# Kernel tuning notes

Measured on AMD Instinct MI355X. Metric: run time of the kernel, lower is better.

The kernel has to match this reference:

```python
import jax, jax.numpy as jnp
import numpy as np

B, L, D, H, MEM, POL = 32, 256, 768, 12, 384, 3
DK = D // H
ALPHA, BETA, GAMA = 1.0, 0.25, 0.1


def _forward(sequence_output, pooled_output, adj_reshape, src_mask, aspect_mask,
             ln_g, ln_b, wq, bq, wk, bk, wd, bd, weight_m, bias_m,
             wa0, ba0, wa1, ba1, ws0, bs0, ws1, bs1, affine1, affine2, wc, bc):
    b, l, d = sequence_output.shape
    h = weight_m.shape[0]
    dk = d // h

    # custom LayerNorm (torch std is unbiased, ddof=1)
    mu = sequence_output.mean(-1, keepdims=True)
    sd = jnp.std(sequence_output, axis=-1, keepdims=True, ddof=1)
    x = ln_g * (sequence_output - mu) / (sd + 1e-6) + ln_b  # gcn_inputs (dropout = eval identity)

    aspect_outs = x * aspect_mask[:, :, None]

    # multi-head projections  [B,H,L,dk]
    q = (x @ wq + bq).reshape(b, l, h, dk).transpose(0, 2, 1, 3)
    k = (x @ wk + bk).reshape(b, l, h, dk).transpose(0, 2, 1, 3)
    asp = aspect_outs @ wd + bd                       # [B,L,dk]
    asp = jnp.broadcast_to(asp[:, None], (b, h, l, dk))

    # aspect-conditioned scores: tanh(aspect @ W_m @ K^T + b_m)   [B,H,L,L]
    asps = jnp.tanh(jnp.einsum('bhld,hde,bhme->bhlm', asp, weight_m, k) + bias_m[0])
    avg = asps.sum(axis=-2) / l                       # [B,H,L]

    # fusion overwrite: for each aspect index idx, row idx and col idx <- avg.
    # Sequential loop semantics (ascending idx, row-then-col) collapse to:
    #   both aspect (i,j): value = avg[min(i,j)];  row-only: avg[j];  col-only: avg[i]
    is_asp = aspect_mask > 0                          # [B,L]
    rowm = is_asp[:, None, :, None]
    colm = is_asp[:, None, None, :]
    avg_i = avg[..., :, None]                         # [B,H,L,1]
    avg_j = avg[..., None, :]                         # [B,H,1,L]
    ge = (jnp.arange(l)[:, None] >= jnp.arange(l)[None, :])  # i>=j -> min=j
    both_val = jnp.where(ge, avg_j, avg_i)
    aspect_scores = jnp.where(rowm & colm, both_val,
                      jnp.where(rowm, avg_j,
                        jnp.where(colm, avg_i, asps)))

    # standard scaled-dot attention
    scores = jnp.einsum('bhld,bhmd->bhlm', q, k) / jnp.sqrt(jnp.float32(dk))
    scores = jnp.where(src_mask[:, None, None, :] == 0, -1e9, scores)
    s_attn = jax.nn.softmax(scores, axis=-1)          # dropout = eval identity

    aspect_score_avg = aspect_scores.mean(axis=1)     # [B,L,L]
    adj_s = s_attn.mean(axis=1)                       # [B,L,L]

    eye = jnp.eye(l, dtype=adj_s.dtype)
    adj_s = adj_s * (1.0 - eye) + eye                 # zero diag then add identity
    adj_s = src_mask[:, :, None] * adj_s

    adj_r = jnp.exp(ALPHA * adj_reshape)
    dist_mask = aspect_score_avg > BETA
    adj_r = jnp.where(dist_mask, 1.0, adj_r)
    adj_ag = adj_r * aspect_score_avg

    log_p = jax.nn.log_softmax(adj_ag, axis=-1)
    log_q = jax.nn.log_softmax(adj_s, axis=-1)
    q_t = jnp.exp(log_q)
    kl = jnp.sum(q_t * (log_q - log_p))
    kl_loss = jnp.exp(-1.0 * kl * GAMA)

    denom_s = adj_s.sum(axis=2, keepdims=True) + 1.0
    denom_ag = adj_ag.sum(axis=2, keepdims=True) + 1.0

    out_ag, out_s = x, x
    was = [(wa0, ba0), (wa1, ba1)]
    wss = [(ws0, bs0), (ws1, bs1)]
    for li in range(2):
        g_ag = jax.nn.relu(((adj_ag @ out_ag) @ was[li][0] + was[li][1]) / denom_ag)
        g_s = jax.nn.relu(((adj_s @ out_s) @ wss[li][0] + wss[li][1]) / denom_s)
        A1 = jax.nn.softmax(jnp.einsum('bld,de,bme->blm', g_ag, affine1, g_s), axis=-1)
        A2 = jax.nn.softmax(jnp.einsum('bld,de,bme->blm', g_s, affine2, g_ag), axis=-1)
        out_ag = A1 @ g_s
        out_s = A2 @ g_ag   # gcn_drop = eval identity

    asp_wn = aspect_mask.sum(axis=1, keepdims=True)   # [B,1]
    m = aspect_mask[:, :, None]
    outputs1 = (out_ag * m).sum(axis=1) / asp_wn      # [B,MEM]
    outputs2 = (out_s * m).sum(axis=1) / asp_wn

    final = jnp.concatenate([outputs1, outputs2, pooled_output], axis=-1) @ wc + bc
    return final, kl_loss


def setup_inputs() -> dict:
    key = jax.random.key(0)
    ks = jax.random.split(key, 16)
    s = 0.02
    pos = jnp.arange(L)
    start = 5 + (jnp.arange(B) % 16)
    aspect_mask = ((pos[None, :] >= start[:, None]) & (pos[None, :] < start[:, None] + 3)).astype(jnp.float32)
    f32 = jnp.float32
    return {
        'sequence_output': jax.random.normal(ks[0], (B, L, D), f32),
        'pooled_output': jax.random.normal(ks[1], (B, D), f32),
        'adj_reshape': jax.random.uniform(ks[2], (B, L, L), f32),
        'src_mask': jnp.ones((B, L), f32),
        'aspect_mask': aspect_mask,
        'ln_g': jnp.ones((D,), f32), 'ln_b': jnp.zeros((D,), f32),
        'wq': jax.random.normal(ks[3], (D, D), f32) * s, 'bq': jnp.zeros((D,), f32),
        'wk': jax.random.normal(ks[4], (D, D), f32) * s, 'bk': jnp.zeros((D,), f32),
        'wd': jax.random.normal(ks[5], (D, DK), f32) * s, 'bd': jnp.zeros((DK,), f32),
        'weight_m': jax.random.normal(ks[6], (H, DK, DK), f32) * s,
        'bias_m': jnp.zeros((1,), f32),
        'wa0': jax.random.normal(ks[7], (D, MEM), f32) * s, 'ba0': jnp.zeros((MEM,), f32),
        'wa1': jax.random.normal(ks[8], (MEM, MEM), f32) * s, 'ba1': jnp.zeros((MEM,), f32),
        'ws0': jax.random.normal(ks[9], (D, MEM), f32) * s, 'bs0': jnp.zeros((MEM,), f32),
        'ws1': jax.random.normal(ks[10], (MEM, MEM), f32) * s, 'bs1': jnp.zeros((MEM,), f32),
        'affine1': jax.random.normal(ks[11], (MEM, MEM), f32) * s,
        'affine2': jax.random.normal(ks[12], (MEM, MEM), f32) * s,
        'wc': jax.random.normal(ks[13], (2 * D, POL), f32) * s, 'bc': jnp.zeros((POL,), f32),
    }


def reference(sequence_output, pooled_output, adj_reshape, src_mask, aspect_mask,
              ln_g, ln_b, wq, bq, wk, bk, wd, bd, weight_m, bias_m,
              wa0, ba0, wa1, ba1, ws0, bs0, ws1, bs1, affine1, affine2, wc, bc):
    return _forward(sequence_output, pooled_output, adj_reshape, src_mask, aspect_mask,
                    ln_g, ln_b, wq, bq, wk, bk, wd, bd, weight_m, bias_m,
                    wa0, ba0, wa1, ba1, ws0, bs0, ws1, bs1, affine1, affine2, wc, bc)
```

## Files before the change

### kernel.cpp

```cpp
#include <hip/hip_runtime.h>

#define B_ 32
#define L_ 256
#define D_ 768
#define H_ 12
#define DK_ 64
#define MEM_ 384

typedef __attribute__((ext_vector_type(8))) short bfrag8;
typedef __attribute__((ext_vector_type(8))) unsigned short us8;
typedef __attribute__((ext_vector_type(4))) float f32x4;

__device__ inline unsigned short f2bf(float f) {
  unsigned u = __float_as_uint(f);
  return (unsigned short)((u + 0x7fffu + ((u >> 16) & 1u)) >> 16);
}
__device__ inline float bf2f(unsigned short u) {
  return __uint_as_float(((unsigned)u) << 16);
}
__device__ inline float tanh_fast(float x) {
  x = fminf(fmaxf(x, -30.f), 30.f);
  float e = __expf(2.f * x);
  return (e - 1.f) * __builtin_amdgcn_rcpf(e + 1.f);
}
__device__ inline void gload_lds16(const unsigned short* g, unsigned short* l) {
  __builtin_amdgcn_global_load_lds(
      (__attribute__((address_space(1))) void*)(g),
      (__attribute__((address_space(3))) void*)(l), 16, 0, 0);
}

__device__ inline float waveRedSum(float v) {
#pragma unroll
  for (int o = 32; o; o >>= 1) v += __shfl_xor(v, o, 64);
  return v;
}
__device__ inline float waveRedMax(float v) {
#pragma unroll
  for (int o = 32; o; o >>= 1) v = fmaxf(v, __shfl_xor(v, o, 64));
  return v;
}
__device__ inline float blkRedSum(float v, float* red) {
  v = waveRedSum(v);
  int w = threadIdx.x >> 6;
  __syncthreads();
  if ((threadIdx.x & 63) == 0) red[w] = v;
  __syncthreads();
  return red[0] + red[1] + red[2] + red[3];
}
__device__ inline float blkRedMax(float v, float* red) {
  v = waveRedMax(v);
  int w = threadIdx.x >> 6;
  __syncthreads();
  if ((threadIdx.x & 63) == 0) red[w] = v;
  __syncthreads();
  return fmaxf(fmaxf(red[0], red[1]), fmaxf(red[2], red[3]));
}

__global__ __launch_bounds__(256) void prep_kernel(
    const float* __restrict__ seq, const float* __restrict__ lng,
    const float* __restrict__ lnb, float* __restrict__ xout,
    unsigned short* __restrict__ xbf,
    const float* __restrict__ wq, unsigned short* __restrict__ wqT,
    const float* __restrict__ wk, unsigned short* __restrict__ wkT,
    const float* __restrict__ wa0, unsigned short* __restrict__ wa0T,
    const float* __restrict__ ws0, unsigned short* __restrict__ ws0T,
    const float* __restrict__ wa1, unsigned short* __restrict__ wa1T,
    const float* __restrict__ ws1, unsigned short* __restrict__ ws1T,
    const float* __restrict__ aff1, unsigned short* __restrict__ aff1T,
    const float* __restrict__ aff2, unsigned short* __restrict__ aff2T,
    const float* __restrict__ wd, unsigned short* __restrict__ wdT,
    const float* __restrict__ wm, unsigned short* __restrict__ wmT) {
  int bid = blockIdx.x;
  if (bid >= 600) {
    long row = bid - 600;
    const float* p = seq + row * D_;
    float v[3];
#pragma unroll
    for (int i = 0; i < 3; ++i) v[i] = p[threadIdx.x + i * 256];
    __shared__ float red[4];
    float s = v[0] + v[1] + v[2];
    s = blkRedSum(s, red);
    float mu = s * (1.f / D_);
    float ss = 0.f;
#pragma unroll
    for (int i = 0; i < 3; ++i) { float d = v[i] - mu; ss += d * d; }
    ss = blkRedSum(ss, red);
    float sd = sqrtf(ss * (1.f / (D_ - 1)));
    float inv = 1.f / (sd + 1e-6f);
#pragma unroll
    for (int i = 0; i < 3; ++i) {
      int c = threadIdx.x + i * 256;
      float o = lng[c] * (v[i] - mu) * inv + lnb[c];
      xout[row * D_ + c] = o;
      xbf[row * D_ + c] = f2bf(o);
    }
    return;
  }
  const float* src; unsigned short* dst; int Rr, Cc, tIdx;
  if (bid < 144)      { src = wq;   dst = wqT;   Rr = 768; Cc = 768; tIdx = bid; }
  else if (bid < 288) { src = wk;   dst = wkT;   Rr = 768; Cc = 768; tIdx = bid - 144; }
  else if (bid < 360) { src = wa0;  dst = wa0T;  Rr = 768; Cc = 384; tIdx = bid - 288; }
  else if (bid < 432) { src = ws0;  dst = ws0T;  Rr = 768; Cc = 384; tIdx = bid - 360; }
  else if (bid < 468) { src = wa1;  dst = wa1T;  Rr = 384; Cc = 384; tIdx = bid - 432; }
  else if (bid < 504) { src = ws1;  dst = ws1T;  Rr = 384; Cc = 384; tIdx = bid - 468; }
  else if (bid < 540) { src = aff1; dst = aff1T; Rr = 384; Cc = 384; tIdx = bid - 504; }
  else if (bid < 576) { src = aff2; dst = aff2T; Rr = 384; Cc = 384; tIdx = bid - 540; }
  else if (bid < 588) { src = wd;   dst = wdT;   Rr = 768; Cc = 64;  tIdx = bid - 576; }
  else { int h = bid - 588; src = wm + h * 4096; dst = wmT + h * 4096; Rr = 64; Cc = 64; tIdx = 0; }
  __shared__ float tile[64][65];
  int nx = Cc >> 6;
  int c0 = (tIdx % nx) * 64, r0 = (tIdx / nx) * 64;
  int tx = threadIdx.x & 63, ty = threadIdx.x >> 6;
#pragma unroll
  for (int i = 0; i < 16; ++i)
    tile[ty + i * 4][tx] = src[(long)(r0 + ty + i * 4) * Cc + c0 + tx];
  __syncthreads();
#pragma unroll
  for (int i = 0; i < 16; ++i)
    dst[(long)(c0 + ty + i * 4) * Rr + r0 + tx] = f2bf(tile[tx][ty + i * 4]);
}

template <int MR>
__global__ __launch_bounds__(256) void gemm_bb(
    const unsigned short* __restrict__ A, const unsigned short* __restrict__ Bt,
    float* __restrict__ C, unsigned short* __restrict__ Cbf,
    unsigned short* __restrict__ CT,
    int M, int N, int K, long sA, long sB, long sC, long sCT,
    const float* __restrict__ bias, const float* __restrict__ rowDiv, int relu,
    const unsigned short* __restrict__ A2, const unsigned short* __restrict__ Bt2,
    float* __restrict__ C2, unsigned short* __restrict__ Cbf2,
    unsigned short* __restrict__ CT2,
    const float* __restrict__ bias2, const float* __restrict__ rowDiv2, int zsplit,
    int GX, int GZ, int gmode) {
  constexpr int MFRAG = MR / 32;
  constexpr int RW = MR / 2;
  constexpr int ASH = MR * 32;
  constexpr int BUFS = ASH + 4096;
  constexpr int TSH = 64 * (MR + 8);
  constexpr int SMN = (2 * BUFS > TSH) ? 2 * BUFS : TSH;
  __shared__ alignas(16) unsigned short smem[SMN];
  const int tid = threadIdx.x;
  int dtot = blockIdx.x;
  int xcd = dtot & 7, rrg = dtot >> 3;
  int gsz = GX * GZ;
  if (gmode == 1) gsz = blockIdx.y;
  int bn, bm, bz;
  if (gmode == 0) {
    int ul = rrg / gsz, j = rrg % gsz;
    bm = ul * 8 + xcd;
    bz = j / GX;
    bn = j % GX;
  } else {
    int gsz2 = GX * GZ;
    int ul = rrg / gsz2, j = rrg % gsz2;
    bz = ul * 8 + xcd;
    bm = j / GX;
    bn = j % GX;
  }
  const unsigned short* Ap = A; const unsigned short* Btp = Bt;
  float* Cp = C; unsigned short* Cbp = Cbf; unsigned short* CTp = CT;
  const float* biasp = bias; const float* rowDivp = rowDiv;
  if (zsplit > 0 && bz >= zsplit) {
    bz -= zsplit;
    Ap = A2; Btp = Bt2; Cp = C2; Cbp = Cbf2; CTp = CT2; biasp = bias2; rowDivp = rowDiv2;
  }
  Ap += (long)bz * sA; Btp += (long)bz * sB;
  if (Cp) Cp += (long)bz * sC;
  if (Cbp) Cbp += (long)bz * sC;
  if (CTp) CTp += (long)bz * sCT;

  f32x4 acc[MFRAG][4] = {};
  const int l = tid & 63, w = tid >> 6;
  const int wr = w >> 1, wc = w & 1;
  const int lr = l & 15, sg = l >> 4;

  const int rc = l >> 2;
  const int sslot = (l & 3) ^ ((rc >> 1) & 3);
  const unsigned short* gA0 = Ap + (long)(bm * MR + w * 16 + rc) * K + sslot * 8;
  const unsigned short* gA1 = (MR == 128)
      ? Ap + (long)(bm * MR + (w + 4) * 16 + rc) * K + sslot * 8 : nullptr;
  const unsigned short* gB0 = Btp + (long)(bn * 128 + w * 16 + rc) * K + sslot * 8;
  const unsigned short* gB1 = Btp + (long)(bn * 128 + (w + 4) * 16 + rc) * K + sslot * 8;
  const int stA0 = w * 512, stA1 = (w + 4) * 512;
  const int stB0 = ASH + w * 512, stB1 = ASH + (w + 4) * 512;

  const int swz = (sg ^ ((lr >> 1) & 3)) * 8;
  int aoff[MFRAG], boff[4];
#pragma unroll
  for (int m = 0; m < MFRAG; ++m) aoff[m] = (wr * RW + m * 16 + lr) * 32 + swz;
#pragma unroll
  for (int n = 0; n < 4; ++n) boff[n] = ASH + (wc * 64 + n * 16 + lr) * 32 + swz;

  const int nt = K >> 5;
  gload_lds16(gA0, smem + stA0);
  if (MR == 128) gload_lds16(gA1, smem + stA1);
  gload_lds16(gB0, smem + stB0);
  gload_lds16(gB1, smem + stB1);

  for (int t = 0; t < nt; ++t) {
    const int cur = (t & 1) * BUFS;
    if (t + 1 < nt) {
      const int nxt = ((t + 1) & 1) * BUFS;
      const int k1 = (t + 1) << 5;
      gload_lds16(gA0 + k1, smem + nxt + stA0);
      if (MR == 128) gload_lds16(gA1 + k1, smem + nxt + stA1);
      gload_lds16(gB0 + k1, smem + nxt + stB0);
      gload_lds16(gB1 + k1, smem + nxt + stB1);
      if constexpr (MR == 128)
        asm volatile("s_waitcnt vmcnt(4)" ::: "memory");
      else
        asm volatile("s_waitcnt vmcnt(3)" ::: "memory");
    } else {
      asm volatile("s_waitcnt vmcnt(0)" ::: "memory");
    }
    __builtin_amdgcn_s_barrier();
    asm volatile("" ::: "memory");
    bfrag8 af[MFRAG], bf[4];
#pragma unroll
    for (int m = 0; m < MFRAG; ++m) af[m] = *(const bfrag8*)(smem + cur + aoff[m]);
#pragma unroll
    for (int n = 0; n < 4; ++n) bf[n] = *(const bfrag8*)(smem + cur + boff[n]);
#pragma unroll
    for (int m = 0; m < MFRAG; ++m)
#pragma unroll
      for (int n = 0; n < 4; ++n)
        acc[m][n] = __builtin_amdgcn_mfma_f32_16x16x32_bf16(af[m], bf[n], acc[m][n], 0, 0, 0);
    asm volatile("" ::: "memory");
    __builtin_amdgcn_s_barrier();
    asm volatile("" ::: "memory");
  }

  if (Cp || Cbp) {
#pragma unroll
    for (int m = 0; m < MFRAG; ++m) {
#pragma unroll
      for (int r = 0; r < 4; ++r) {
        int row = bm * MR + wr * RW + m * 16 + (l >> 4) * 4 + r;
        float rd = rowDivp ? 1.f / rowDivp[(long)bz * M + row] : 1.f;
#pragma unroll
        for (int n = 0; n < 4; ++n) {
          int col = bn * 128 + wc * 64 + n * 16 + lr;
          float v = acc[m][n][r];
          if (biasp) v += biasp[col];
          v *= rd;
          if (relu) v = fmaxf(v, 0.f);
          if (Cp) Cp[(long)row * N + col] = v;
          if (Cbp) Cbp[(long)row * N + col] = f2bf(v);
        }
      }
    }
  }
  if (CT) {
    auto Ts = (unsigned short(*)[MR + 8])smem;
#pragma unroll
    for (int ch = 0; ch < 2; ++ch) {
      __syncthreads();
      if (wc == ch) {
#pragma unroll
        for (int m = 0; m < MFRAG; ++m) {
#pragma unroll
          for (int r = 0; r < 4; ++r) {
            int rowl = wr * RW + m * 16 + (l >> 4) * 4 + r;
            float rd = rowDivp ? 1.f / rowDivp[(long)bz * M + bm * MR + rowl] : 1.f;
#pragma unroll
            for (int n = 0; n < 4; ++n) {
              int col = bn * 128 + wc * 64 + n * 16 + lr;
              float v = acc[m][n][r];
              if (biasp) v += biasp[col];
              v *= rd;
              if (relu) v = fmaxf(v, 0.f);
              Ts[n * 16 + lr][rowl] = f2bf(v);
            }
          }
        }
      }
      __syncthreads();
      int trow = tid >> 2, tc = (tid & 3) * (MR / 4);
      int colg = bn * 128 + ch * 64 + trow;
      int rowg = bm * MR + tc;
      unsigned short* dp = CTp + (long)(rowg >> 8) * sCT + (long)colg * 256 + (rowg & 255);
#pragma unroll
      for (int j = 0; j < MR / 32; ++j)
        *(us8*)(dp + j * 8) = *(const us8*)&Ts[trow][tc + j * 8];
    }
  }
}

__global__ __launch_bounds__(256) void attn_asp(
    const unsigned short* __restrict__ qbf, const unsigned short* __restrict__ kbf,
    const float* __restrict__ srcm,
    float* __restrict__ part0, float* __restrict__ part1,
    const unsigned short* __restrict__ xbf, const unsigned short* __restrict__ wdT,
    const float* __restrict__ amask, const float* __restrict__ bd,
    unsigned short* __restrict__ aspbf) {
  int t = threadIdx.x;
  int w = t >> 6, l = t & 63;
  int lr = l & 15, kg = (l >> 4) * 8;
  if (blockIdx.x >= 1024) {
    int l0 = (blockIdx.x - 1024) << 4;
    const unsigned short* ap = xbf + (long)(l0 + lr) * D_ + kg;
    const unsigned short* bp = wdT + (long)(w * 16 + lr) * D_ + kg;
    f32x4 acc = {};
#pragma unroll
    for (int k0 = 0; k0 < D_; k0 += 32) {
      bfrag8 af = *(const bfrag8*)(ap + k0);
      bfrag8 bf = *(const bfrag8*)(bp + k0);
      acc = __builtin_amdgcn_mfma_f32_16x16x32_bf16(af, bf, acc, 0, 0, 0);
    }
    int col = w * 16 + lr;
#pragma unroll
    for (int r = 0; r < 4; ++r) {
      int row = l0 + (l >> 4) * 4 + r;
      float v = acc[r] * amask[row] + bd[col];
      aspbf[(long)row * DK_ + col] = f2bf(v);
    }
    return;
  }
  int d = blockIdx.x;
  int b = (d & 7) + 8 * ((d >> 3) & 3);
  int rest = d >> 5;
  int l0 = (rest & 15) << 4;
  int half = rest >> 4;
  int rbase = (l >> 4) * 4;
  __shared__ float red[3][2][16][4];
  float acc[4][4] = {};
  float cmv[4];
#pragma unroll
  for (int ct = 0; ct < 4; ++ct) cmv[ct] = srcm[b * L_ + w * 64 + ct * 16 + lr];

  const int hp0 = half * 3;
  const long qrow = (long)b * L_ + l0 + lr;
  const unsigned short* apq = qbf + qrow * D_ + hp0 * 128 + kg;
  bfrag8 a00 = *(const bfrag8*)apq;
  bfrag8 a01 = *(const bfrag8*)(apq + 32);
  bfrag8 a10 = *(const bfrag8*)(apq + 64);
  bfrag8 a11 = *(const bfrag8*)(apq + 96);
  bfrag8 kv[4][4];
#pragma unroll
  for (int ct = 0; ct < 4; ++ct) {
    const unsigned short* bp =
        kbf + ((long)b * L_ + w * 64 + ct * 16 + lr) * D_ + hp0 * 128 + kg;
    kv[ct][0] = *(const bfrag8*)bp;
    kv[ct][1] = *(const bfrag8*)(bp + 32);
    kv[ct][2] = *(const bfrag8*)(bp + 64);
    kv[ct][3] = *(const bfrag8*)(bp + 96);
  }

#pragma unroll 1
  for (int ph = 0; ph < 3; ++ph) {
    float sv0[4][4], sv1[4][4];
#pragma unroll
    for (int ct = 0; ct < 4; ++ct) {
      f32x4 c0 = {}, c1 = {};
      c0 = __builtin_amdgcn_mfma_f32_16x16x32_bf16(a00, kv[ct][0], c0, 0, 0, 0);
      c0 = __builtin_amdgcn_mfma_f32_16x16x32_bf16(a01, kv[ct][1], c0, 0, 0, 0);
      c1 = __builtin_amdgcn_mfma_f32_16x16x32_bf16(a10, kv[ct][2], c1, 0, 0, 0);
      c1 = __builtin_amdgcn_mfma_f32_16x16x32_bf16(a11, kv[ct][3], c1, 0, 0, 0);
#pragma unroll
      for (int r = 0; r < 4; ++r) { sv0[ct][r] = c0[r]; sv1[ct][r] = c1[r]; }
    }
    if (ph < 2) {
      const unsigned short* apn = qbf + qrow * D_ + (hp0 + ph + 1) * 128 + kg;
      a00 = *(const bfrag8*)apn;
      a01 = *(const bfrag8*)(apn + 32);
      a10 = *(const bfrag8*)(apn + 64);
      a11 = *(const bfrag8*)(apn + 96);
#pragma unroll
      for (int ct = 0; ct < 4; ++ct) {
        const unsigned short* bp =
            kbf + ((long)b * L_ + w * 64 + ct * 16 + lr) * D_ + (hp0 + ph + 1) * 128 + kg;
        kv[ct][0] = *(const bfrag8*)bp;
        kv[ct][1] = *(const bfrag8*)(bp + 32);
        kv[ct][2] = *(const bfrag8*)(bp + 64);
        kv[ct][3] = *(const bfrag8*)(bp + 96);
      }
    }
#pragma unroll
    for (int ct = 0; ct < 4; ++ct) {
      bool msk = (cmv[ct] == 0.f);
#pragma unroll
      for (int r = 0; r < 4; ++r) {
        sv0[ct][r] = __expf(msk ? -1e9f : sv0[ct][r] * 0.125f);
        sv1[ct][r] = __expf(msk ? -1e9f : sv1[ct][r] * 0.125f);
      }
    }
#pragma unroll
    for (int r = 0; r < 4; ++r) {
      float s0 = sv0[0][r] + sv0[1][r] + sv0[2][r] + sv0[3][r];
      float s1 = sv1[0][r] + sv1[1][r] + sv1[2][r] + sv1[3][r];
#pragma unroll
      for (int o = 1; o < 16; o <<= 1) {
        s0 += __shfl_xor(s0, o, 64);
        s1 += __shfl_xor(s1, o, 64);
      }
      if (lr == 0) {
        red[ph][0][rbase + r][w] = s0;
        red[ph][1][rbase + r][w] = s1;
      }
    }
    __syncthreads();
#pragma unroll
    for (int r = 0; r < 4; ++r) {
      f32x4 s4 = *(const f32x4*)&red[ph][0][rbase + r][0];
      float inv0 = __builtin_amdgcn_rcpf(s4[0] + s4[1] + s4[2] + s4[3] + 1e-30f);
      f32x4 t4 = *(const f32x4*)&red[ph][1][rbase + r][0];
      float inv1 = __builtin_amdgcn_rcpf(t4[0] + t4[1] + t4[2] + t4[3] + 1e-30f);
#pragma unroll
      for (int ct = 0; ct < 4; ++ct)
        acc[ct][r] += sv0[ct][r] * inv0 + sv1[ct][r] * inv1;
    }
  }

  float* pp = half ? part1 : part0;
#pragma unroll
  for (int r = 0; r < 4; ++r) {
    int row = l0 + rbase + r;
#pragma unroll
    for (int ct = 0; ct < 4; ++ct) {
      int col = w * 64 + ct * 16 + lr;
      pp[((long)b * L_ + row) * L_ + col] = acc[ct][r];
    }
  }
}

__global__ __launch_bounds__(256) void asp_wm_v2(const unsigned short* __restrict__ aspbf,
                                                 const unsigned short* __restrict__ wmT,
                                                 unsigned short* __restrict__ tmpA) {
  int bh = blockIdx.x;
  int b = bh / H_, h = bh % H_;
  int t = threadIdx.x;
  int w = t >> 6, l = t & 63;
  int lr = l & 15, kg = (l >> 4) * 8;
  const unsigned short* wp = wmT + h * 4096;
  f32x4 acc[4][4] = {};
#pragma unroll
  for (int ks = 0; ks < 2; ++ks) {
    int k0 = ks * 32;
    bfrag8 af[4], bf[4];
#pragma unroll
    for (int m = 0; m < 4; ++m)
      af[m] = *(const bfrag8*)(aspbf + (long)(b * L_ + w * 64 + m * 16 + lr) * DK_ + k0 + kg);
#pragma unroll
    for (int n = 0; n < 4; ++n)
      bf[n] = *(const bfrag8*)(wp + (n * 16 + lr) * 64 + k0 + kg);
#pragma unroll
    for (int m = 0; m < 4; ++m)
#pragma unroll
      for (int n = 0; n < 4; ++n)
        acc[m][n] = __builtin_amdgcn_mfma_f32_16x16x32_bf16(af[m], bf[n], acc[m][n], 0, 0, 0);
  }
#pragma unroll
  for (int m = 0; m < 4; ++m)
#pragma unroll
    for (int n = 0; n < 4; ++n)
#pragma unroll
      for (int r = 0; r < 4; ++r) {
        int row = w * 64 + m * 16 + (l >> 4) * 4 + r;
        int col = n * 16 + lr;
        tmpA[(((long)b * H_ + h) * L_ + row) * DK_ + col] = f2bf(acc[m][n][r]);
      }
}

__global__ __launch_bounds__(256) void gemm_sfmx(
    const unsigned short* __restrict__ u1, const unsigned short* __restrict__ g1,
    unsigned short* __restrict__ P1,
    const unsigned short* __restrict__ u2, const unsigned short* __restrict__ g2,
    unsigned short* __restrict__ P2) {
  constexpr int ASH = 64 * 32;
  constexpr int BUFS = ASH + 8192;
  __shared__ alignas(16) unsigned short smem[2 * BUFS];
  __shared__ float redm[2][64];
  __shared__ float reds[2][64];
  int dtot = blockIdx.x;
  int xcd = dtot & 7, rr = dtot >> 3;
  int bm = rr & 3;
  int bz = (rr >> 2) * 8 + xcd;
  const unsigned short* Ap; const unsigned short* Bp; unsigned short* Pp;
  if (bz < 32) {
    Ap = u1 + (long)bz * L_ * MEM_; Bp = g1 + (long)bz * L_ * MEM_;
    Pp = P1 + (long)bz * L_ * L_;
  } else {
    int z = bz - 32;
    Ap = u2 + (long)z * L_ * MEM_; Bp = g2 + (long)z * L_ * MEM_;
    Pp = P2 + (long)z * L_ * L_;
  }
  const int t = threadIdx.x;
  const int l = t & 63, w = t >> 6;
  const int wr = w >> 1, wc = w & 1;
  const int lr = l & 15, sg = l >> 4;
  f32x4 acc[2][8] = {};

  const int rc = l >> 2;
  const int sslot = (l & 3) ^ ((rc >> 1) & 3);
  const unsigned short* gA = Ap + (long)(bm * 64 + w * 16 + rc) * MEM_ + sslot * 8;
  const unsigned short* gB[4];
#pragma unroll
  for (int j = 0; j < 4; ++j)
    gB[j] = Bp + (long)(w * 64 + j * 16 + rc) * MEM_ + sslot * 8;
  const int stA = w * 512;
  int stB[4];
#pragma unroll
  for (int j = 0; j < 4; ++j) stB[j] = ASH + (w * 4 + j) * 512;

  const int swz = (sg ^ ((lr >> 1) & 3)) * 8;
  int aoff[2], boff[8];
#pragma unroll
  for (int m = 0; m < 2; ++m) aoff[m] = (wr * 32 + m * 16 + lr) * 32 + swz;
#pragma unroll
  for (int n = 0; n < 8; ++n) boff[n] = ASH + (wc * 128 + n * 16 + lr) * 32 + swz;

  gload_lds16(gA, smem + stA);
#pragma unroll
  for (int j = 0; j < 4; ++j) gload_lds16(gB[j], smem + stB[j]);

  constexpr int NT = MEM_ / 32;
  for (int tt = 0; tt < NT; ++tt) {
    const int cur = (tt & 1) * BUFS;
    if (tt + 1 < NT) {
      const int nxt = ((tt + 1) & 1) * BUFS;
      const int k1 = (tt + 1) << 5;
      gload_lds16(gA + k1, smem + nxt + stA);
#pragma unroll
      for (int j = 0; j < 4; ++j) gload_lds16(gB[j] + k1, smem + nxt + stB[j]);
      asm volatile("s_waitcnt vmcnt(5)" ::: "memory");
    } else {
      asm volatile("s_waitcnt vmcnt(0)" ::: "memory");
    }
    __builtin_amdgcn_s_barrier();
    asm volatile("" ::: "memory");
    bfrag8 af[2], bf[8];
#pragma unroll
    for (int m = 0; m < 2; ++m) af[m] = *(const bfrag8*)(smem + cur + aoff[m]);
#pragma unroll
    for (int n = 0; n < 8; ++n) bf[n] = *(const bfrag8*)(smem + cur + boff[n]);
#pragma unroll
    for (int m = 0; m < 2; ++m)
#pragma unroll
      for (int n = 0; n < 8; ++n)
        acc[m][n] = __builtin_amdgcn_mfma_f32_16x16x32_bf16(af[m], bf[n], acc[m][n], 0, 0, 0);
    asm volatile("" ::: "memory");
    __builtin_amdgcn_s_barrier();
    asm volatile("" ::: "memory");
  }

#pragma unroll
  for (int m = 0; m < 2; ++m) {
#pragma unroll
    for (int r = 0; r < 4; ++r) {
      int lrow = wr * 32 + m * 16 + (l >> 4) * 4 + r;
      float mx = -1e30f;
#pragma unroll
      for (int n = 0; n < 8; ++n) mx = fmaxf(mx, acc[m][n][r]);
#pragma unroll
      for (int o = 1; o < 16; o <<= 1) mx = fmaxf(mx, __shfl_xor(mx, o, 64));
      if (lr == 0) redm[wc][lrow] = mx;
    }
  }
  __syncthreads();
#pragma unroll
  for (int m = 0; m < 2; ++m) {
#pragma unroll
    for (int r = 0; r < 4; ++r) {
      int lrow = wr * 32 + m * 16 + (l >> 4) * 4 + r;
      float mx = fmaxf(redm[0][lrow], redm[1][lrow]);
      float s = 0.f;
#pragma unroll
      for (int n = 0; n < 8; ++n) {
        float e = __expf(acc[m][n][r] - mx);
        acc[m][n][r] = e;
        s += e;
      }
#pragma unroll
      for (int o = 1; o < 16; o <<= 1) s += __shfl_xor(s, o, 64);
      if (lr == 0) reds[wc][lrow] = s;
    }
  }
  __syncthreads();
#pragma unroll
  for (int m = 0; m < 2; ++m) {
#pragma unroll
    for (int r = 0; r < 4; ++r) {
      int lrow = wr * 32 + m * 16 + (l >> 4) * 4 + r;
      float inv = 1.f / (reds[0][lrow] + reds[1][lrow]);
      int row = bm * 64 + lrow;
#pragma unroll
      for (int n = 0; n < 8; ++n) {
        int col = wc * 128 + n * 16 + lr;
        Pp[(long)row * L_ + col] = f2bf(acc[m][n][r] * inv);
      }
    }
  }
}

__global__ __launch_bounds__(256) void asps_mean_v2(
    const unsigned short* __restrict__ tmpA,
    const unsigned short* __restrict__ kbf,
    const float* __restrict__ bias_m,
    float* __restrict__ asps_mean) {
  int blk = blockIdx.x;
  int b = blk >> 4, l0 = (blk & 15) << 4;
  int t = threadIdx.x;
  int w = t >> 6, l = t & 63;
  int lr = l & 15, kg = (l >> 4) * 8;
  float bm = bias_m[0];
  float accg[4][4] = {};
  for (int h = 0; h < H_; ++h) {
    const unsigned short* ap = tmpA + (((long)b * H_ + h) * L_ + l0 + lr) * 64 + kg;
    bfrag8 af0 = *(const bfrag8*)ap;
    bfrag8 af1 = *(const bfrag8*)(ap + 32);
#pragma unroll
    for (int ct = 0; ct < 4; ++ct) {
      const unsigned short* bp =
          kbf + ((long)b * L_ + w * 64 + ct * 16 + lr) * D_ + h * 64 + kg;
      bfrag8 bf0 = *(const bfrag8*)bp;
      bfrag8 bf1 = *(const bfrag8*)(bp + 32);
      f32x4 accl = {};
      accl = __builtin_amdgcn_mfma_f32_16x16x32_bf16(af0, bf0, accl, 0, 0, 0);
      accl = __builtin_amdgcn_mfma_f32_16x16x32_bf16(af1, bf1, accl, 0, 0, 0);
#pragma unroll
      for (int r = 0; r < 4; ++r) accg[ct][r] += tanh_fast(accl[r] + bm);
    }
  }
#pragma unroll
  for (int ct = 0; ct < 4; ++ct) {
    int col = w * 64 + ct * 16 + lr;
#pragma unroll
    for (int r = 0; r < 4; ++r) {
      int row = l0 + (l >> 4) * 4 + r;
      asps_mean[((long)b * L_ + row) * L_ + col] = accg[ct][r] * (1.f / H_);
    }
  }
}

__global__ __launch_bounds__(1024) void avgh_kernel(const float* __restrict__ asps_mean,
                                                    float* __restrict__ avgH) {
  int b = blockIdx.x;
  int m = threadIdx.x & 255, q = threadIdx.x >> 8;
  __shared__ float part[4][256];
  float s = 0.f;
  for (int l = q * 64; l < q * 64 + 64; ++l)
    s += asps_mean[((long)b * L_ + l) * L_ + m];
  part[q][m] = s;
  __syncthreads();
  if (q == 0)
    avgH[b * L_ + m] = (part[0][m] + part[1][m] + part[2][m] + part[3][m]) * (1.f / L_);
}

__global__ __launch_bounds__(256) void adjag_kl(const float* __restrict__ part0,
                                                const float* __restrict__ part1,
                                                const float* __restrict__ srcm,
                                                const float* __restrict__ asps_mean,
                                                const float* __restrict__ avgH,
                                                const float* __restrict__ amask,
                                                const float* __restrict__ adjr,
                                                unsigned short* __restrict__ adjsbf,
                                                unsigned short* __restrict__ adjagbf,
                                                float* __restrict__ klpart,
                                                float* __restrict__ den_s,
                                                float* __restrict__ den_ag) {
  long row = blockIdx.x;
  int m = threadIdx.x;
  int l = (int)(row & 255);
  int b = (int)(row >> 8);
  long idx = row * L_ + m;
  float s = (part0[idx] + part1[idx]) * (1.f / H_);
  if (m == l) s = 1.f;
  s *= srcm[b * L_ + l];
  adjsbf[idx] = f2bf(s);
  bool rowa = amask[b * L_ + l] > 0.f;
  bool cola = amask[b * L_ + m] > 0.f;
  float asa;
  if (rowa && cola) asa = (l >= m) ? avgH[b * L_ + m] : avgH[b * L_ + l];
  else if (rowa)    asa = avgH[b * L_ + m];
  else if (cola)    asa = avgH[b * L_ + l];
  else              asa = asps_mean[idx];
  float r = (asa > 0.25f) ? 1.f : expf(adjr[idx]);
  float a = r * asa;
  adjagbf[idx] = f2bf(a);

  __shared__ float red[4];
  float sum_s = blkRedSum(s, red);
  float sum_a = blkRedSum(a, red);
  float mx_s = blkRedMax(s, red);
  float mx_a = blkRedMax(a, red);
  float es = expf(s - mx_s), ea = expf(a - mx_a);
  float ses = blkRedSum(es, red);
  float sea = blkRedSum(ea, red);
  float logq = (s - mx_s) - logf(ses);
  float logp = (a - mx_a) - logf(sea);
  float term = (es / ses) * (logq - logp);
  float kp = blkRedSum(term, red);
  if (m == 0) {
    klpart[row] = kp;
    den_s[row] = sum_s + 1.f;
    den_ag[row] = sum_a + 1.f;
  }
}

__global__ __launch_bounds__(256) void final_kernel(const unsigned short* __restrict__ o_ag,
                                                    const unsigned short* __restrict__ o_s,
                                                    const float* __restrict__ pooled,
                                                    const float* __restrict__ amask,
                                                    const float* __restrict__ wc,
                                                    const float* __restrict__ bc,
                                                    const float* __restrict__ klpart,
                                                    float* __restrict__ dout) {
  int b = blockIdx.x, t = threadIdx.x;
  __shared__ float red[4];
  if (b == B_) {
    float s = 0.f;
    for (int i = t; i < B_ * L_; i += 256) s += klpart[i];
    s = blkRedSum(s, red);
    if (t == 0) dout[96] = expf(-s * 0.1f);
    return;
  }
  __shared__ float cS[1536];
  __shared__ float maskS[256];
  maskS[t] = amask[b * L_ + t];
  float wn = blkRedSum(maskS[t], red);
  for (int e = t; e < MEM_; e += 256) {
    float s1 = 0.f, s2 = 0.f;
    for (int l = 0; l < L_; ++l) {
      float mk = maskS[l];
      if (mk != 0.f) {
        s1 += mk * bf2f(o_ag[((long)b * L_ + l) * MEM_ + e]);
        s2 += mk * bf2f(o_s[((long)b * L_ + l) * MEM_ + e]);
      }
    }
    cS[e] = s1 / wn;
    cS[MEM_ + e] = s2 / wn;
  }
  for (int j = t; j < D_; j += 256) cS[2 * MEM_ + j] = pooled[b * D_ + j];
  __syncthreads();
  float p0 = 0.f, p1 = 0.f, p2 = 0.f;
  for (int j = t; j < 1536; j += 256) {
    float v = cS[j];
    p0 += v * wc[j * 3 + 0];
    p1 += v * wc[j * 3 + 1];
    p2 += v * wc[j * 3 + 2];
  }
  p0 = blkRedSum(p0, red);
  p1 = blkRedSum(p1, red);
  p2 = blkRedSum(p2, red);
  if (t == 0) {
    dout[b * 3 + 0] = p0 + bc[0];
    dout[b * 3 + 1] = p1 + bc[1];
    dout[b * 3 + 2] = p2 + bc[2];
  }
}

extern "C" void kernel_launch(void* const* d_in, const int* in_sizes, int n_in,
                              void* d_out, int out_size, void* d_ws, size_t ws_size,
                              hipStream_t stream) {
  const float* seq    = (const float*)d_in[0];
  const float* pooled = (const float*)d_in[1];
  const float* adjr   = (const float*)d_in[2];
  const float* srcm   = (const float*)d_in[3];
  const float* amask  = (const float*)d_in[4];
  const float* ln_g   = (const float*)d_in[5];
  const float* ln_b   = (const float*)d_in[6];
  const float* wq     = (const float*)d_in[7];
  const float* bq     = (const float*)d_in[8];
  const float* wk     = (const float*)d_in[9];
  const float* bk     = (const float*)d_in[10];
  const float* wd     = (const float*)d_in[11];
  const float* bd     = (const float*)d_in[12];
  const float* wm     = (const float*)d_in[13];
  const float* bm     = (const float*)d_in[14];
  const float* wa0    = (const float*)d_in[15];
  const float* ba0    = (const float*)d_in[16];
  const float* wa1    = (const float*)d_in[17];
  const float* ba1    = (const float*)d_in[18];
  const float* ws0    = (const float*)d_in[19];
  const float* bs0    = (const float*)d_in[20];
  const float* ws1    = (const float*)d_in[21];
  const float* bs1    = (const float*)d_in[22];
  const float* aff1   = (const float*)d_in[23];
  const float* aff2   = (const float*)d_in[24];
  const float* wc     = (const float*)d_in[25];
  const float* bc     = (const float*)d_in[26];

  float* ws = (float*)d_ws;
  float* S0 = ws;
  float* S1 = S0 + 6291456;
  float* S2 = S1 + 3145728;
  float* S3 = S2 + 3145728;
  float* S4 = S3 + 3145728;
  float* S5 = S4 + 524288;
  float* part0  = S5 + 2097152;
  float* part1  = part0 + 2097152;
  unsigned short* adjsbf  = (unsigned short*)(part1 + 2097152);
  unsigned short* adjagbf = adjsbf + 2097152;
  unsigned short* wT      = adjagbf + 2097152;
  unsigned short* wqT   = wT;
  unsigned short* wkT   = wT + 589824;
  unsigned short* wa0T  = wT + 1179648;
  unsigned short* ws0T  = wT + 1474560;
  unsigned short* wa1T  = wT + 1769472;
  unsigned short* ws1T  = wT + 1916928;
  unsigned short* aff1T = wT + 2064384;
  unsigned short* aff2T = wT + 2211840;
  float* tail   = (float*)(wT + 2359296);
  float* avgH   = tail;
  float* den_s  = avgH + 8192;
  float* den_ag = den_s + 8192;
  float* klp    = den_ag + 8192;

  float* x = S0;
  unsigned short* o_agbf = (unsigned short*)S0;
  unsigned short* o_sbf  = o_agbf + 3145728;
  unsigned short* gTag   = o_agbf + 6291456;
  unsigned short* gTs    = o_agbf + 9437184;
  unsigned short* xbf    = (unsigned short*)S1;
  unsigned short* qbf    = (unsigned short*)S2;
  unsigned short* tmpA   = (unsigned short*)S2;
  unsigned short* g_agbf = (unsigned short*)S2;
  unsigned short* g_sbf  = g_agbf + 3145728;
  unsigned short* kbf    = (unsigned short*)S3;
  unsigned short* tTag   = (unsigned short*)S3;
  unsigned short* tTs    = tTag + 3145728;
  unsigned short* u1bf   = (unsigned short*)S3;
  unsigned short* u2bf   = u1bf + 3145728;
  unsigned short* aspbf  = (unsigned short*)S4;
  unsigned short* wdT    = aspbf + 524288;
  unsigned short* wmT    = wdT + 49152;
  float* asps = S5;
  unsigned short* P1bf = (unsigned short*)S5;
  unsigned short* P2bf = P1bf + 2097152;
  float* dout = (float*)d_out;

  const long sAdjSh = (long)L_ * L_;
  const long sMemSh = (long)L_ * MEM_;

  prep_kernel<<<600 + B_ * L_, 256, 0, stream>>>(
      seq, ln_g, ln_b, x, xbf, wq, wqT, wk, wkT, wa0, wa0T, ws0, ws0T,
      wa1, wa1T, ws1, ws1T, aff1, aff1T, aff2, aff2T, wd, wdT, wm, wmT);
  gemm_bb<128><<<768, 256, 0, stream>>>(
      xbf, wqT, nullptr, qbf, nullptr, 8192, 768, 768, 0, 0, 0, 0, bq, nullptr, 0,
      xbf, wkT, nullptr, kbf, nullptr, bk, nullptr, 1, 6, 2, 0);
  attn_asp<<<1536, 256, 0, stream>>>(qbf, kbf, srcm, part0, part1,
                                     xbf, wdT, amask, bd, aspbf);
  asp_wm_v2<<<B_ * H_, 256, 0, stream>>>(aspbf, wmT, tmpA);
  asps_mean_v2<<<B_ * 16, 256, 0, stream>>>(tmpA, kbf, bm, asps);
  avgh_kernel<<<B_, 1024, 0, stream>>>(asps, avgH);
  adjag_kl<<<B_ * L_, 256, 0, stream>>>(part0, part1, srcm, asps, avgH, amask, adjr,
                                        adjsbf, adjagbf, klp, den_s, den_ag);

  for (int li = 0; li < 2; ++li) {
    int Kd = li ? MEM_ : D_;
    const unsigned short* inag = li ? o_agbf : xbf;
    const unsigned short* ins  = li ? o_sbf : xbf;
    const unsigned short* wAT = li ? wa1T : wa0T;
    const float* bA = li ? ba1 : ba0;
    const unsigned short* wST = li ? ws1T : ws0T;
    const float* bS = li ? bs1 : bs0;
    gemm_bb<64><<<768, 256, 0, stream>>>(
        inag, wAT, nullptr, nullptr, tTag, 8192, MEM_, Kd, 0, 0, 0, sMemSh,
        nullptr, nullptr, 0,
        ins, wST, nullptr, nullptr, tTs, nullptr, nullptr, 1, 3, 2, 0);
    gemm_bb<64><<<768, 256, 0, stream>>>(
        adjagbf, tTag, nullptr, g_agbf, gTag, L_, MEM_, L_, sAdjSh, sMemSh, sMemSh,
        sMemSh, bA, den_ag, 1,
        adjsbf, tTs, nullptr, g_sbf, gTs, bS, den_s, 32, 3, 4, 1);
    gemm_bb<64><<<768, 256, 0, stream>>>(
        g_agbf, aff1T, nullptr, u1bf, nullptr, 8192, MEM_, MEM_, 0, 0, 0, 0,
        nullptr, nullptr, 0,
        g_sbf, aff2T, nullptr, u2bf, nullptr, nullptr, nullptr, 1, 3, 2, 0);
    gemm_sfmx<<<256, 256, 0, stream>>>(u1bf, g_sbf, P1bf, u2bf, g_agbf, P2bf);
    gemm_bb<64><<<768, 256, 0, stream>>>(
        P1bf, gTs, nullptr, o_agbf, nullptr, L_, MEM_, L_, sAdjSh, sMemSh, sMemSh, 0,
        nullptr, nullptr, 0,
        P2bf, gTag, nullptr, o_sbf, nullptr, nullptr, nullptr, 32, 3, 4, 1);
  }

  final_kernel<<<B_ + 1, 256, 0, stream>>>(o_agbf, o_sbf, pooled, amask, wc, bc,
                                           klp, dout);
}
```

Measured before the change: 361.5 us.

## Triple-buffer LDS prefetch in GEMM kernels and halve Q/K GEMM row tile

Both gemm_bb and gemm_sfmx move from double-buffered to triple-buffered LDS staging. Each loads two K-tiles ahead and relaxes the vmcnt waits so global-to-LDS copies overlap more compute. The Q/K projection launch also switches from a 128-row to a 64-row tile with twice as many blocks, which raises parallelism. The cost is more LDS per block, which may lower occupancy, plus a dead gmode==1 gsz path is removed.

Result: no change. 362.4 us (+0.3%).

```diff
diff --git a/kernel.cpp b/kernel.cpp
--- a/kernel.cpp
+++ b/kernel.cpp
@@ -137,15 +137,14 @@
   constexpr int ASH = MR * 32;
   constexpr int BUFS = ASH + 4096;
   constexpr int TSH = 64 * (MR + 8);
-  constexpr int SMN = (2 * BUFS > TSH) ? 2 * BUFS : TSH;
+  constexpr int SMN = (3 * BUFS > TSH) ? 3 * BUFS : TSH;
   __shared__ alignas(16) unsigned short smem[SMN];
   const int tid = threadIdx.x;
   int dtot = blockIdx.x;
   int xcd = dtot & 7, rrg = dtot >> 3;
-  int gsz = GX * GZ;
-  if (gmode == 1) gsz = blockIdx.y;
   int bn, bm, bz;
   if (gmode == 0) {
+    int gsz = GX * GZ;
     int ul = rrg / gsz, j = rrg % gsz;
     bm = ul * 8 + xcd;
     bz = j / GX;
@@ -192,20 +191,33 @@
   for (int n = 0; n < 4; ++n) boff[n] = ASH + (wc * 64 + n * 16 + lr) * 32 + swz;
 
   const int nt = K >> 5;
-  gload_lds16(gA0, smem + stA0);
-  if (MR == 128) gload_lds16(gA1, smem + stA1);
-  gload_lds16(gB0, smem + stB0);
-  gload_lds16(gB1, smem + stB1);
-
+  {
+    gload_lds16(gA0, smem + stA0);
+    if (MR == 128) gload_lds16(gA1, smem + stA1);
+    gload_lds16(gB0, smem + stB0);
+    gload_lds16(gB1, smem + stB1);
+    const int k1 = 32;
+    gload_lds16(gA0 + k1, smem + BUFS + stA0);
+    if (MR == 128) gload_lds16(gA1 + k1, smem + BUFS + stA1);
+    gload_lds16(gB0 + k1, smem + BUFS + stB0);
+    gload_lds16(gB1 + k1, smem + BUFS + stB1);
+  }
+
+  int bidx = 0, nidx = 2;
   for (int t = 0; t < nt; ++t) {
-    const int cur = (t & 1) * BUFS;
-    if (t + 1 < nt) {
-      const int nxt = ((t + 1) & 1) * BUFS;
-      const int k1 = (t + 1) << 5;
-      gload_lds16(gA0 + k1, smem + nxt + stA0);
-      if (MR == 128) gload_lds16(gA1 + k1, smem + nxt + stA1);
-      gload_lds16(gB0 + k1, smem + nxt + stB0);
-      gload_lds16(gB1 + k1, smem + nxt + stB1);
+    const int cur = bidx * BUFS;
+    if (t + 2 < nt) {
+      const int nxt = nidx * BUFS;
+      const int k2 = (t + 2) << 5;
+      gload_lds16(gA0 + k2, smem + nxt + stA0);
+      if (MR == 128) gload_lds16(gA1 + k2, smem + nxt + stA1);
+      gload_lds16(gB0 + k2, smem + nxt + stB0);
+      gload_lds16(gB1 + k2, smem + nxt + stB1);
+      if constexpr (MR == 128)
+        asm volatile("s_waitcnt vmcnt(8)" ::: "memory");
+      else
+        asm volatile("s_waitcnt vmcnt(6)" ::: "memory");
+    } else if (t + 1 < nt) {
       if constexpr (MR == 128)
         asm volatile("s_waitcnt vmcnt(4)" ::: "memory");
       else
@@ -228,6 +240,8 @@
     asm volatile("" ::: "memory");
     __builtin_amdgcn_s_barrier();
     asm volatile("" ::: "memory");
+    bidx = (bidx == 2) ? 0 : bidx + 1;
+    nidx = (nidx == 2) ? 0 : nidx + 1;
   }
 
   if (Cp || Cbp) {
@@ -468,7 +482,7 @@
     unsigned short* __restrict__ P2) {
   constexpr int ASH = 64 * 32;
   constexpr int BUFS = ASH + 8192;
-  __shared__ alignas(16) unsigned short smem[2 * BUFS];
+  __shared__ alignas(16) unsigned short smem[3 * BUFS];
   __shared__ float redm[2][64];
   __shared__ float reds[2][64];
   int dtot = blockIdx.x;
@@ -512,16 +526,22 @@
   gload_lds16(gA, smem + stA);
 #pragma unroll
   for (int j = 0; j < 4; ++j) gload_lds16(gB[j], smem + stB[j]);
+  gload_lds16(gA + 32, smem + BUFS + stA);
+#pragma unroll
+  for (int j = 0; j < 4; ++j) gload_lds16(gB[j] + 32, smem + BUFS + stB[j]);
 
   constexpr int NT = MEM_ / 32;
+  int bidx = 0, nidx = 2;
   for (int tt = 0; tt < NT; ++tt) {
-    const int cur = (tt & 1) * BUFS;
-    if (tt + 1 < NT) {
-      const int nxt = ((tt + 1) & 1) * BUFS;
-      const int k1 = (tt + 1) << 5;
-      gload_lds16(gA + k1, smem + nxt + stA);
-#pragma unroll
-      for (int j = 0; j < 4; ++j) gload_lds16(gB[j] + k1, smem + nxt + stB[j]);
+    const int cur = bidx * BUFS;
+    if (tt + 2 < NT) {
+      const int nxt = nidx * BUFS;
+      const int k2 = (tt + 2) << 5;
+      gload_lds16(gA + k2, smem + nxt + stA);
+#pragma unroll
+      for (int j = 0; j < 4; ++j) gload_lds16(gB[j] + k2, smem + nxt + stB[j]);
+      asm volatile("s_waitcnt vmcnt(10)" ::: "memory");
+    } else if (tt + 1 < NT) {
       asm volatile("s_waitcnt vmcnt(5)" ::: "memory");
     } else {
       asm volatile("s_waitcnt vmcnt(0)" ::: "memory");
@@ -541,6 +561,8 @@
     asm volatile("" ::: "memory");
     __builtin_amdgcn_s_barrier();
     asm volatile("" ::: "memory");
+    bidx = (bidx == 2) ? 0 : bidx + 1;
+    nidx = (nidx == 2) ? 0 : nidx + 1;
   }
 
 #pragma unroll
@@ -835,7 +857,7 @@
   prep_kernel<<<600 + B_ * L_, 256, 0, stream>>>(
       seq, ln_g, ln_b, x, xbf, wq, wqT, wk, wkT, wa0, wa0T, ws0, ws0T,
       wa1, wa1T, ws1, ws1T, aff1, aff1T, aff2, aff2T, wd, wdT, wm, wmT);
-  gemm_bb<128><<<768, 256, 0, stream>>>(
+  gemm_bb<64><<<1536, 256, 0, stream>>>(
       xbf, wqT, nullptr, qbf, nullptr, 8192, 768, 768, 0, 0, 0, 0, bq, nullptr, 0,
       xbf, wkT, nullptr, kbf, nullptr, bk, nullptr, 1, 6, 2, 0);
   attn_asp<<<1536, 256, 0, stream>>>(qbf, kbf, srcm, part0, part1,
```

## Fuse affine projection GEMM into the score-softmax kernel

Applied to the files above, without the earlier changes.

Removes the separate GEMM that computed u = g @ affine (written to global as bf16) and instead computes each 64-row tile of u inside the softmax kernel, in two 192-column halves held in LDS, reading A and the affine weights directly from global. This saves one launch per layer and a round trip of the u intermediate through memory. In exchange each block recomputes its u tile using uncached direct global loads of the weights without LDS staging, and the in-loop recompute at tile 6 serializes with the main pipeline, so the kernel, launched with only 256 blocks, may become compute- or latency-bound.

Measured after the change: 444.1 us. +22.9%, slower.

```diff
diff --git a/kernel.cpp b/kernel.cpp
--- a/kernel.cpp
+++ b/kernel.cpp
@@ -142,10 +142,9 @@
   const int tid = threadIdx.x;
   int dtot = blockIdx.x;
   int xcd = dtot & 7, rrg = dtot >> 3;
-  int gsz = GX * GZ;
-  if (gmode == 1) gsz = blockIdx.y;
   int bn, bm, bz;
   if (gmode == 0) {
+    int gsz = GX * GZ;
     int ul = rrg / gsz, j = rrg % gsz;
     bm = ul * 8 + xcd;
     bz = j / GX;
@@ -461,78 +460,102 @@
       }
 }
 
-__global__ __launch_bounds__(256) void gemm_sfmx(
-    const unsigned short* __restrict__ u1, const unsigned short* __restrict__ g1,
-    unsigned short* __restrict__ P1,
-    const unsigned short* __restrict__ u2, const unsigned short* __restrict__ g2,
-    unsigned short* __restrict__ P2) {
-  constexpr int ASH = 64 * 32;
-  constexpr int BUFS = ASH + 8192;
-  __shared__ alignas(16) unsigned short smem[2 * BUFS];
+__global__ __launch_bounds__(256) void gemm_usfmx(
+    const unsigned short* __restrict__ g_a1, const unsigned short* __restrict__ g_b1,
+    const unsigned short* __restrict__ aff1T, const unsigned short* __restrict__ aff2T,
+    unsigned short* __restrict__ P1, unsigned short* __restrict__ P2) {
+  constexpr int BSH = 8192;
+  __shared__ unsigned short Us[64][200];
+  __shared__ alignas(16) unsigned short Bs[2 * BSH];
   __shared__ float redm[2][64];
   __shared__ float reds[2][64];
   int dtot = blockIdx.x;
   int xcd = dtot & 7, rr = dtot >> 3;
   int bm = rr & 3;
   int bz = (rr >> 2) * 8 + xcd;
-  const unsigned short* Ap; const unsigned short* Bp; unsigned short* Pp;
+  const unsigned short* Ag; const unsigned short* Bg; const unsigned short* afT;
+  unsigned short* Pp;
   if (bz < 32) {
-    Ap = u1 + (long)bz * L_ * MEM_; Bp = g1 + (long)bz * L_ * MEM_;
-    Pp = P1 + (long)bz * L_ * L_;
+    Ag = g_a1 + (long)bz * L_ * MEM_; Bg = g_b1 + (long)bz * L_ * MEM_;
+    afT = aff1T; Pp = P1 + (long)bz * L_ * L_;
   } else {
     int z = bz - 32;
-    Ap = u2 + (long)z * L_ * MEM_; Bp = g2 + (long)z * L_ * MEM_;
-    Pp = P2 + (long)z * L_ * L_;
+    Ag = g_b1 + (long)z * L_ * MEM_; Bg = g_a1 + (long)z * L_ * MEM_;
+    afT = aff2T; Pp = P2 + (long)z * L_ * L_;
   }
   const int t = threadIdx.x;
   const int l = t & 63, w = t >> 6;
   const int wr = w >> 1, wc = w & 1;
-  const int lr = l & 15, sg = l >> 4;
-  f32x4 acc[2][8] = {};
+  const int lr = l & 15, sg = l >> 4, kg = sg * 8;
 
   const int rc = l >> 2;
   const int sslot = (l & 3) ^ ((rc >> 1) & 3);
-  const unsigned short* gA = Ap + (long)(bm * 64 + w * 16 + rc) * MEM_ + sslot * 8;
   const unsigned short* gB[4];
 #pragma unroll
   for (int j = 0; j < 4; ++j)
-    gB[j] = Bp + (long)(w * 64 + j * 16 + rc) * MEM_ + sslot * 8;
-  const int stA = w * 512;
+    gB[j] = Bg + (long)(w * 64 + j * 16 + rc) * MEM_ + sslot * 8;
   int stB[4];
 #pragma unroll
-  for (int j = 0; j < 4; ++j) stB[j] = ASH + (w * 4 + j) * 512;
+  for (int j = 0; j < 4; ++j) stB[j] = (w * 4 + j) * 512;
+
+#pragma unroll
+  for (int j = 0; j < 4; ++j) gload_lds16(gB[j], Bs + stB[j]);
+
+  const unsigned short* arow = Ag + (long)(bm * 64 + w * 16 + lr) * MEM_ + kg;
+  auto computeU = [&](int h) {
+    f32x4 uacc[12] = {};
+    for (int k0 = 0; k0 < MEM_; k0 += 32) {
+      bfrag8 af = *(const bfrag8*)(arow + k0);
+#pragma unroll
+      for (int n = 0; n < 12; ++n) {
+        bfrag8 bf =
+            *(const bfrag8*)(afT + (long)(h * 192 + n * 16 + lr) * MEM_ + k0 + kg);
+        uacc[n] = __builtin_amdgcn_mfma_f32_16x16x32_bf16(af, bf, uacc[n], 0, 0, 0);
+      }
+    }
+#pragma unroll
+    for (int n = 0; n < 12; ++n)
+#pragma unroll
+      for (int r = 0; r < 4; ++r)
+        Us[w * 16 + sg * 4 + r][n * 16 + lr] = f2bf(uacc[n][r]);
+  };
+
+  computeU(0);
+  __syncthreads();
 
   const int swz = (sg ^ ((lr >> 1) & 3)) * 8;
-  int aoff[2], boff[8];
-#pragma unroll
-  for (int m = 0; m < 2; ++m) aoff[m] = (wr * 32 + m * 16 + lr) * 32 + swz;
-#pragma unroll
-  for (int n = 0; n < 8; ++n) boff[n] = ASH + (wc * 128 + n * 16 + lr) * 32 + swz;
-
-  gload_lds16(gA, smem + stA);
-#pragma unroll
-  for (int j = 0; j < 4; ++j) gload_lds16(gB[j], smem + stB[j]);
-
+  int aoffr[2], boff[8];
+#pragma unroll
+  for (int m = 0; m < 2; ++m) aoffr[m] = (wr * 32 + m * 16 + lr) * 200 + kg;
+#pragma unroll
+  for (int n = 0; n < 8; ++n) boff[n] = (wc * 128 + n * 16 + lr) * 32 + swz;
+
+  f32x4 acc[2][8] = {};
   constexpr int NT = MEM_ / 32;
   for (int tt = 0; tt < NT; ++tt) {
-    const int cur = (tt & 1) * BUFS;
+    if (tt == 6) {
+      computeU(1);
+      __syncthreads();
+    }
+    const int cur = (tt & 1) * BSH;
     if (tt + 1 < NT) {
-      const int nxt = ((tt + 1) & 1) * BUFS;
+      const int nxt = ((tt + 1) & 1) * BSH;
       const int k1 = (tt + 1) << 5;
-      gload_lds16(gA + k1, smem + nxt + stA);
-#pragma unroll
-      for (int j = 0; j < 4; ++j) gload_lds16(gB[j] + k1, smem + nxt + stB[j]);
-      asm volatile("s_waitcnt vmcnt(5)" ::: "memory");
+#pragma unroll
+      for (int j = 0; j < 4; ++j) gload_lds16(gB[j] + k1, Bs + nxt + stB[j]);
+      asm volatile("s_waitcnt vmcnt(4)" ::: "memory");
     } else {
       asm volatile("s_waitcnt vmcnt(0)" ::: "memory");
     }
     __builtin_amdgcn_s_barrier();
     asm volatile("" ::: "memory");
+    const int kk = (tt >= 6 ? tt - 6 : tt) << 5;
     bfrag8 af[2], bf[8];
 #pragma unroll
-    for (int m = 0; m < 2; ++m) af[m] = *(const bfrag8*)(smem + cur + aoff[m]);
-#pragma unroll
-    for (int n = 0; n < 8; ++n) bf[n] = *(const bfrag8*)(smem + cur + boff[n]);
+    for (int m = 0; m < 2; ++m)
+      af[m] = *(const bfrag8*)(&Us[0][0] + aoffr[m] + kk);
+#pragma unroll
+    for (int n = 0; n < 8; ++n) bf[n] = *(const bfrag8*)(Bs + cur + boff[n]);
 #pragma unroll
     for (int m = 0; m < 2; ++m)
 #pragma unroll
@@ -819,8 +842,6 @@
   unsigned short* kbf    = (unsigned short*)S3;
   unsigned short* tTag   = (unsigned short*)S3;
   unsigned short* tTs    = tTag + 3145728;
-  unsigned short* u1bf   = (unsigned short*)S3;
-  unsigned short* u2bf   = u1bf + 3145728;
   unsigned short* aspbf  = (unsigned short*)S4;
   unsigned short* wdT    = aspbf + 524288;
   unsigned short* wmT    = wdT + 49152;
@@ -862,11 +883,7 @@
         adjagbf, tTag, nullptr, g_agbf, gTag, L_, MEM_, L_, sAdjSh, sMemSh, sMemSh,
         sMemSh, bA, den_ag, 1,
         adjsbf, tTs, nullptr, g_sbf, gTs, bS, den_s, 32, 3, 4, 1);
-    gemm_bb<64><<<768, 256, 0, stream>>>(
-        g_agbf, aff1T, nullptr, u1bf, nullptr, 8192, MEM_, MEM_, 0, 0, 0, 0,
-        nullptr, nullptr, 0,
-        g_sbf, aff2T, nullptr, u2bf, nullptr, nullptr, nullptr, 1, 3, 2, 0);
-    gemm_sfmx<<<256, 256, 0, stream>>>(u1bf, g_sbf, P1bf, u2bf, g_agbf, P2bf);
+    gemm_usfmx<<<256, 256, 0, stream>>>(g_agbf, g_sbf, aff1T, aff2T, P1bf, P2bf);
     gemm_bb<64><<<768, 256, 0, stream>>>(
         P1bf, gTs, nullptr, o_agbf, nullptr, L_, MEM_, L_, sAdjSh, sMemSh, sMemSh, 0,
         nullptr, nullptr, 0,
```
